# Optimization experiments

Hardware: AMD Instinct MI355X
Metric: run time of the kernel (lower is better)

The kernel has to match this reference:

```python
import jax, jax.numpy as jnp
import numpy as np

B, N, T, F = 8, 2000, 64, 32
H = 128    # lstm_hidden
GH = 128   # gnn_hidden
E = 32000  # edges


def setup_inputs() -> dict:
    key = jax.random.key(0)
    ks = jax.random.split(key, 12)
    s = 0.05
    return {
        "x": jax.random.normal(ks[0], (B, N, T, F), jnp.float32),
        "edge_index": jax.random.randint(ks[1], (2, E), 0, N, dtype=jnp.int32),
        # LSTM params (torch gate order i, f, g, o)
        "Wih": jax.random.normal(ks[2], (4 * H, F), jnp.float32) * s,
        "Whh": jax.random.normal(ks[3], (4 * H, H), jnp.float32) * s,
        "bih": jax.random.normal(ks[4], (4 * H,), jnp.float32) * s,
        "bhh": jax.random.normal(ks[5], (4 * H,), jnp.float32) * s,
        # GCNConv params
        "gcn_W": jax.random.normal(ks[6], (H, GH), jnp.float32) * s,
        "gcn_b": jax.random.normal(ks[7], (GH,), jnp.float32) * s,
        # shared MLP head
        "mlp_W1": jax.random.normal(ks[8], (GH, GH // 2), jnp.float32) * s,
        "mlp_b1": jax.random.normal(ks[9], (GH // 2,), jnp.float32) * s,
        "mlp_W2": jax.random.normal(ks[10], (GH // 2, 1), jnp.float32) * s,
        "mlp_b2": jax.random.normal(ks[11], (1,), jnp.float32) * s,
    }


def _lstm_last_h(x, Wih, Whh, bih, bhh):
    # x: [M, T, F] -> last hidden state [M, H]
    M = x.shape[0]
    xg = jnp.einsum('mtf,gf->mtg', x, Wih) + bih  # precompute input gates [M, T, 4H]

    def step(carry, xg_t):
        h, c = carry
        z = xg_t + h @ Whh.T + bhh
        i, f, g, o = jnp.split(z, 4, axis=-1)
        i = jax.nn.sigmoid(i)
        f = jax.nn.sigmoid(f)
        g = jnp.tanh(g)
        o = jax.nn.sigmoid(o)
        c = f * c + i * g
        h = o * jnp.tanh(c)
        return (h, c), None

    h0 = jnp.zeros((M, H), x.dtype)
    c0 = jnp.zeros((M, H), x.dtype)
    (h, _), _ = jax.lax.scan(step, (h0, c0), jnp.swapaxes(xg, 0, 1))
    return h


def reference(x, edge_index, Wih, Whh, bih, bhh, gcn_W, gcn_b,
              mlp_W1, mlp_b1, mlp_W2, mlp_b2):
    Bx, Nx, Tx, Fx = x.shape
    # LSTM over all B*N node sequences, take last hidden state
    h = _lstm_last_h(x.reshape(Bx * Nx, Tx, Fx), Wih, Whh, bih, bhh)
    node_features = h.reshape(Bx, Nx, H)

    # GCNConv (PyG semantics): add self-loops, symmetric normalization
    loops = jnp.arange(Nx, dtype=edge_index.dtype)
    src = jnp.concatenate([edge_index[0], loops])
    dst = jnp.concatenate([edge_index[1], loops])
    deg = jnp.zeros((Nx,), x.dtype).at[dst].add(1.0)
    dinv = jnp.where(deg > 0, jax.lax.rsqrt(deg), 0.0)
    norm = dinv[src] * dinv[dst]  # [E+N]

    xw = node_features @ gcn_W                     # [B, N, GH]
    msgs = xw[:, src, :] * norm[None, :, None]     # gather + scale [B, E+N, GH]
    agg = jnp.zeros((Bx, Nx, GH), x.dtype).at[:, dst, :].add(msgs) + gcn_b

    # shared MLP head (dropout is identity in eval mode)
    h1 = jax.nn.silu(agg @ mlp_W1 + mlp_b1)
    out = h1 @ mlp_W2 + mlp_b2                     # [B, N, 1]
    return out.squeeze(-1)                         # [B, N]
```

## Files before the change

kernel.cpp:

```cpp
#include <hip/hip_runtime.h>

typedef _Float16 f16x8 __attribute__((ext_vector_type(8)));
typedef _Float16 f16x4 __attribute__((ext_vector_type(4)));
typedef _Float16 f16x2 __attribute__((ext_vector_type(2)));
typedef float f32x4 __attribute__((ext_vector_type(4)));

#define NB_   8
#define NN_   2000
#define TT_   64
#define FF_   32
#define HH_   128
#define EE_   32000
#define KD    160
#define RSTR  192
#define GELEM (32*RSTR)

__device__ __forceinline__ float fexp2(float v) { return __builtin_amdgcn_exp2f(v); }
__device__ __forceinline__ float frcp(float v)  { return __builtin_amdgcn_rcpf(v); }

__global__ void prep_kernel(const float* __restrict__ Wih, const float* __restrict__ Whh,
                            const float* __restrict__ bih, const float* __restrict__ bhh,
                            const float* __restrict__ gcnW,
                            _Float16* __restrict__ W16, _Float16* __restrict__ Wg16,
                            float* __restrict__ bias, float* __restrict__ deg) {
  int idx = blockIdx.x * 256 + threadIdx.x;
  if (idx < 512 * KD) {
    int col = idx / KD, k = idx % KD;
    float v = (k < 32) ? Wih[col * 32 + k] : Whh[col * 128 + (k - 32)];
    float sc = (col >= 256 && col < 384) ? -2.88539008f : -1.44269504f;
    W16[idx] = (_Float16)(v * sc);
  } else if (idx < 512 * KD + 128 * 128) {
    int i2 = idx - 512 * KD;
    int colg = i2 >> 7, k = i2 & 127;
    Wg16[i2] = (_Float16)gcnW[k * 128 + colg];
  } else if (idx < 512 * KD + 128 * 128 + 512) {
    int i3 = idx - (512 * KD + 128 * 128);
    float sc = (i3 >= 256 && i3 < 384) ? -2.88539008f : -1.44269504f;
    bias[i3] = (bih[i3] + bhh[i3]) * sc;
  } else if (idx < 512 * KD + 128 * 128 + 512 + NN_) {
    deg[idx - (512 * KD + 128 * 128 + 512)] = 0.f;
  }
}

__global__ void deg_kernel(const int* __restrict__ ei, float* __restrict__ deg) {
  int e = blockIdx.x * 256 + threadIdx.x;
  if (e < EE_ + NN_) {
    int d = (e < EE_) ? ei[EE_ + e] : (e - EE_);
    atomicAdd(&deg[d], 1.f);
  }
}

__global__ void dinv_kernel(const float* __restrict__ deg, float* __restrict__ dinv) {
  int n = blockIdx.x * 256 + threadIdx.x;
  if (n < NN_) {
    float d = deg[n];
    dinv[n] = (d > 0.f) ? __builtin_amdgcn_rsqf(d) : 0.f;
  }
}

__global__ void scan_kernel(const float* __restrict__ deg, int* __restrict__ offs,
                            int* __restrict__ cursor) {
  __shared__ int s0[2048], s1[2048];
  int t = threadIdx.x;
  for (int i = t; i < 2048; i += 1024) s0[i] = (i < NN_) ? ((int)deg[i] - 1) : 0;
  __syncthreads();
  int* src = s0; int* dst = s1;
  for (int off = 1; off < 2048; off <<= 1) {
    for (int i = t; i < 2048; i += 1024)
      dst[i] = src[i] + ((i >= off) ? src[i - off] : 0);
    __syncthreads();
    int* tmp = src; src = dst; dst = tmp;
  }
  for (int i = t; i < NN_; i += 1024) {
    int exc = src[i] - ((int)deg[i] - 1);
    offs[i] = exc;
    cursor[i] = exc;
  }
}

__global__ void fill_kernel(const int* __restrict__ ei, const float* __restrict__ dinv,
                            int* __restrict__ cursor, int* __restrict__ csr_src,
                            float* __restrict__ csr_w) {
  int e = blockIdx.x * 256 + threadIdx.x;
  if (e >= EE_) return;
  int s = ei[e], d = ei[EE_ + e];
  int pos = atomicAdd(&cursor[d], 1);
  csr_src[pos] = s;
  csr_w[pos] = dinv[s] * dinv[d];
}

__global__ __launch_bounds__(512, 2) void lstm_gcn_kernel(
    const float* __restrict__ x, const _Float16* __restrict__ W16,
    const float* __restrict__ bias, const _Float16* __restrict__ Wg16,
    float* __restrict__ xw) {
  __shared__ _Float16 A[64 * RSTR];
  const int tid  = threadIdx.x;
  const int wave = tid >> 6;
  const int lane = tid & 63;
  const int n15  = lane & 15;
  const int q    = lane >> 4;
  const int m    = n15 & 7;
  const int hm   = m >> 2;
  const int qx   = q ^ (m & 3);
  const int node0 = blockIdx.x * 64;

  f16x8 Af[4][5];
  float4 bgv[4];
#pragma unroll
  for (int g = 0; g < 4; ++g) {
    const int row = g * 128 + wave * 16 + n15;
#pragma unroll
    for (int kc = 0; kc < 5; ++kc)
      Af[g][kc] = *(const f16x8*)(W16 + row * KD + kc * 32 + q * 8);
    bgv[g] = *(const float4*)(bias + g * 128 + wave * 16 + q * 4);
  }

  const int bRow = n15 * RSTR + (qx << 3);
  const int hOff = n15 * RSTR + (((4 + 2 * wave + (q >> 1)) ^ m) << 3) + ((q & 1) << 2);

  const int xrow = tid >> 4;
  const int xf   = (tid & 15) * 2;
  const int xOff = xrow * RSTR + (((xf >> 3) ^ (xrow & 7)) << 3) + (xf & 7);
  const float* xb0 = x + (size_t)(node0 + xrow) * (TT_ * FF_) + xf;
  const float* xb1 = x + (size_t)(node0 + 32 + xrow) * (TT_ * FF_) + xf;

  for (int i = tid; i < 1024; i += 512) {
    int row = i >> 4, ci = i & 15;
    f16x8 z8 = {(_Float16)0, (_Float16)0, (_Float16)0, (_Float16)0,
                (_Float16)0, (_Float16)0, (_Float16)0, (_Float16)0};
    *(f16x8*)(A + row * RSTR + (((4 + ci) ^ (row & 7)) << 3)) = z8;
  }
  {
    float2 v0 = *(const float2*)xb0;
    float2 v1 = *(const float2*)xb1;
    f16x2 p0 = {(_Float16)v0.x, (_Float16)v0.y};
    f16x2 p1 = {(_Float16)v1.x, (_Float16)v1.y};
    *(f16x2*)(A + xOff) = p0;
    *(f16x2*)(A + GELEM + xOff) = p1;
  }
  __syncthreads();

  f32x4 accX[2][4], accY[2][4], cX[2], cY[2];
#pragma unroll
  for (int nt = 0; nt < 2; ++nt) { cX[nt] = (f32x4){0,0,0,0}; cY[nt] = (f32x4){0,0,0,0}; }

  auto mfma_half = [&](int G, int nt, f32x4 (&acc)[4]) {
#pragma unroll
    for (int g = 0; g < 4; ++g)
      acc[g] = (f32x4){bgv[g].x, bgv[g].y, bgv[g].z, bgv[g].w};
#pragma unroll
    for (int kc = 0; kc < 5; ++kc) {
      f16x8 bf = *(const f16x8*)(A + G + nt * (16 * RSTR) + bRow + ((kc ^ hm) << 5));
#pragma unroll
      for (int g = 0; g < 4; ++g)
        acc[g] = __builtin_amdgcn_mfma_f32_16x16x32_f16(Af[g][kc], bf, acc[g], 0, 0, 0);
    }
  };

  auto gates_half = [&](int G, int nt, f32x4 (&acc)[4], f32x4& c) {
    const float EM = 2.68435456e8f;
    float so[4], eC[4], dC[4];
#pragma unroll
    for (int r = 0; r < 4; ++r) {
      float ei = fminf(fexp2(acc[0][r]), EM);
      float ef = fminf(fexp2(acc[1][r]), EM);
      float eg = fminf(fexp2(acc[2][r]), EM);
      float eo = fminf(fexp2(acc[3][r]), EM);
      float di = 1.f + ei, df = 1.f + ef, dg = 1.f + eg, dd = 1.f + eo;
      float p0 = di * df, p1 = dg * dd;
      float rP = frcp(p0 * p1);
      float r0 = rP * p1, r1 = rP * p0;
      float si = r0 * df, sf = r0 * di;
      float tg = 2.f * (r1 * dd) - 1.f;
      so[r] = r1 * dg;
      c[r] = sf * c[r] + si * tg;
    }
#pragma unroll
    for (int r = 0; r < 4; ++r) {
      eC[r] = fminf(fexp2(-2.88539008f * c[r]), EM);
      dC[r] = 1.f + eC[r];
    }
    float q0 = dC[0] * dC[1], q1 = dC[2] * dC[3];
    float rQ = frcp(q0 * q1);
    float s0 = rQ * q1, s1 = rQ * q0;
    f16x4 hp = {(_Float16)(so[0] * (2.f * (s0 * dC[1]) - 1.f)),
                (_Float16)(so[1] * (2.f * (s0 * dC[0]) - 1.f)),
                (_Float16)(so[2] * (2.f * (s1 * dC[3]) - 1.f)),
                (_Float16)(so[3] * (2.f * (s1 * dC[2]) - 1.f))};
    *(f16x4*)(A + G + nt * (16 * RSTR) + hOff) = hp;
  };

  mfma_half(0, 0, accX[0]);
  mfma_half(0, 1, accX[1]);
  __syncthreads();

  for (int t = 0; t < TT_; ++t) {
    const bool more = (t + 1 < TT_);
    {
      float2 xv;
      if (more) xv = *(const float2*)(xb0 + (t + 1) * FF_);
      mfma_half(GELEM, 0, accY[0]);
      gates_half(0, 0, accX[0], cX[0]);
      mfma_half(GELEM, 1, accY[1]);
      gates_half(0, 1, accX[1], cX[1]);
      if (more) { f16x2 p = {(_Float16)xv.x, (_Float16)xv.y}; *(f16x2*)(A + xOff) = p; }
    }
    __syncthreads();
    {
      float2 xv;
      if (more) xv = *(const float2*)(xb1 + (t + 1) * FF_);
      if (more) mfma_half(0, 0, accX[0]);
      gates_half(GELEM, 0, accY[0], cY[0]);
      if (more) mfma_half(0, 1, accX[1]);
      gates_half(GELEM, 1, accY[1], cY[1]);
      if (more) { f16x2 p = {(_Float16)xv.x, (_Float16)xv.y}; *(f16x2*)(A + GELEM + xOff) = p; }
    }
    __syncthreads();
  }

  f16x8 Ag[4];
#pragma unroll
  for (int kc = 0; kc < 4; ++kc)
    Ag[kc] = *(const f16x8*)(Wg16 + (wave * 16 + n15) * HH_ + kc * 32 + q * 8);
  f32x4 acc2[4];
#pragma unroll
  for (int nt = 0; nt < 4; ++nt) acc2[nt] = (f32x4){0, 0, 0, 0};
#pragma unroll
  for (int kc = 0; kc < 4; ++kc)
#pragma unroll
    for (int nt = 0; nt < 4; ++nt) {
      f16x8 bf = *(const f16x8*)(A + (nt * 16 + n15) * RSTR +
                                 (((kc + 1) ^ hm) << 5) + (qx << 3));
      acc2[nt] = __builtin_amdgcn_mfma_f32_16x16x32_f16(Ag[kc], bf, acc2[nt], 0, 0, 0);
    }
#pragma unroll
  for (int nt = 0; nt < 4; ++nt)
    *(float4*)(xw + (size_t)(node0 + nt * 16 + n15) * HH_ + wave * 16 + q * 4) =
        (float4){acc2[nt][0], acc2[nt][1], acc2[nt][2], acc2[nt][3]};
}

__global__ void gathermlp_kernel(const float* __restrict__ xw, const int* __restrict__ offs,
                                 const float* __restrict__ deg, const float* __restrict__ dinv,
                                 const int* __restrict__ csr_src, const float* __restrict__ csr_w,
                                 const float* __restrict__ gcnb,
                                 const float* __restrict__ W1, const float* __restrict__ b1,
                                 const float* __restrict__ W2, const float* __restrict__ b2,
                                 float* __restrict__ out) {
  __shared__ float aggs[8][128];
  const int d = blockIdx.x;
  const int tid = threadIdx.x;
  {
    const int j  = tid & 127;
    const int bh = tid >> 7;
    const int beg = offs[d];
    const int cnt = (int)deg[d] - 1;
    const size_t bbase = (size_t)(bh * 4) * NN_ * 128;
    float a0 = 0.f, a1 = 0.f, a2 = 0.f, a3 = 0.f;
    for (int e = 0; e < cnt; ++e) {
      int s   = csr_src[beg + e];
      float w = csr_w[beg + e];
      const float* p = xw + bbase + (size_t)s * 128 + j;
      a0 += w * p[0];
      a1 += w * p[NN_ * 128];
      a2 += w * p[2 * NN_ * 128];
      a3 += w * p[3 * NN_ * 128];
    }
    {
      float di = dinv[d];
      float w = di * di;
      const float* p = xw + bbase + (size_t)d * 128 + j;
      a0 += w * p[0];
      a1 += w * p[NN_ * 128];
      a2 += w * p[2 * NN_ * 128];
      a3 += w * p[3 * NN_ * 128];
    }
    float bj = gcnb[j];
    aggs[bh * 4 + 0][j] = a0 + bj;
    aggs[bh * 4 + 1][j] = a1 + bj;
    aggs[bh * 4 + 2][j] = a2 + bj;
    aggs[bh * 4 + 3][j] = a3 + bj;
  }
  __syncthreads();
  const int b = tid >> 5;
  const int t = tid & 31;
  float acc1 = b1[t], acc2 = b1[t + 32];
#pragma unroll 4
  for (int k = 0; k < 128; ++k) {
    float a = aggs[b][k];
    acc1 += a * W1[k * 64 + t];
    acc2 += a * W1[k * 64 + t + 32];
  }
  float s1 = acc1 * frcp(1.f + fexp2(-1.44269504f * acc1));
  float s2 = acc2 * frcp(1.f + fexp2(-1.44269504f * acc2));
  float part = s1 * W2[t] + s2 * W2[t + 32];
#pragma unroll
  for (int msk = 16; msk >= 1; msk >>= 1) part += __shfl_xor(part, msk);
  if (t == 0) out[(size_t)b * NN_ + d] = part + b2[0];
}

extern "C" void kernel_launch(void* const* d_in, const int* in_sizes, int n_in,
                              void* d_out, int out_size, void* d_ws, size_t ws_size,
                              hipStream_t stream) {
  const float* x    = (const float*)d_in[0];
  const int*   ei   = (const int*)d_in[1];
  const float* Wih  = (const float*)d_in[2];
  const float* Whh  = (const float*)d_in[3];
  const float* bih  = (const float*)d_in[4];
  const float* bhh  = (const float*)d_in[5];
  const float* gcnW = (const float*)d_in[6];
  const float* gcnb = (const float*)d_in[7];
  const float* W1   = (const float*)d_in[8];
  const float* b1   = (const float*)d_in[9];
  const float* W2   = (const float*)d_in[10];
  const float* b2   = (const float*)d_in[11];
  float* out = (float*)d_out;
  char* ws = (char*)d_ws;

  _Float16* W16    = (_Float16*)(ws);
  _Float16* Wg16   = (_Float16*)(ws + 163840);
  float*    bias   = (float*)(ws + 196608);
  float*    xw     = (float*)(ws + 198656);
  float*    deg    = (float*)(ws + 8390656);
  float*    dinv   = (float*)(ws + 8398848);
  int*      offs   = (int*)(ws + 8407040);
  int*      cursor = (int*)(ws + 8415232);
  int*      csrs   = (int*)(ws + 8423424);
  float*    csrw   = (float*)(ws + 8551424);

  prep_kernel<<<394, 256, 0, stream>>>(Wih, Whh, bih, bhh, gcnW, W16, Wg16, bias, deg);
  deg_kernel<<<133, 256, 0, stream>>>(ei, deg);
  dinv_kernel<<<8, 256, 0, stream>>>(deg, dinv);
  scan_kernel<<<1, 1024, 0, stream>>>(deg, offs, cursor);
  fill_kernel<<<125, 256, 0, stream>>>(ei, dinv, cursor, csrs, csrw);
  lstm_gcn_kernel<<<250, 512, 0, stream>>>(x, W16, bias, Wg16, xw);
  gathermlp_kernel<<<NN_, 256, 0, stream>>>(xw, offs, deg, dinv, csrs, csrw,
                                            gcnb, W1, b1, W2, b2, out);
}
```

Baseline: 423.6 us.

## Halve LSTM nodes per block, move input weights to LDS, transpose xw for gather

The LSTM kernel now handles 32 nodes per block instead of 64 and launches 500 blocks with a higher occupancy target. It drops the two-group ping-pong software pipeline, keeps the input-projection weights and bias in LDS rather than registers, and uses plain per-gate sigmoid/tanh instead of shared-reciprocal tricks. The xw output is stored node-major with batch interleaved so each gather touches one contiguous 4KB row. The MLP gets a transposed W1 in LDS with float4 dot products and an edge loop unrolled by two, and the dinv kernel is folded into the scan kernel. The trade is more waves available to hide latency against losing the explicit MFMA/gate overlap, plus extra per-block LDS traffic for weights and for staging W1.

```diff
diff --git a/kernel.cpp b/kernel.cpp
--- a/kernel.cpp
+++ b/kernel.cpp
@@ -13,7 +13,8 @@
 #define EE_   32000
 #define KD    160
 #define RSTR  192
-#define GELEM (32*RSTR)
+#define NODES 32
+#define WXSTR 40
 
 __device__ __forceinline__ float fexp2(float v) { return __builtin_amdgcn_exp2f(v); }
 __device__ __forceinline__ float frcp(float v)  { return __builtin_amdgcn_rcpf(v); }
@@ -50,16 +51,8 @@
   }
 }
 
-__global__ void dinv_kernel(const float* __restrict__ deg, float* __restrict__ dinv) {
-  int n = blockIdx.x * 256 + threadIdx.x;
-  if (n < NN_) {
-    float d = deg[n];
-    dinv[n] = (d > 0.f) ? __builtin_amdgcn_rsqf(d) : 0.f;
-  }
-}
-
 __global__ void scan_kernel(const float* __restrict__ deg, int* __restrict__ offs,
-                            int* __restrict__ cursor) {
+                            int* __restrict__ cursor, float* __restrict__ dinv) {
   __shared__ int s0[2048], s1[2048];
   int t = threadIdx.x;
   for (int i = t; i < 2048; i += 1024) s0[i] = (i < NN_) ? ((int)deg[i] - 1) : 0;
@@ -75,6 +68,8 @@
     int exc = src[i] - ((int)deg[i] - 1);
     offs[i] = exc;
     cursor[i] = exc;
+    float d = deg[i];
+    dinv[i] = (d > 0.f) ? __builtin_amdgcn_rsqf(d) : 0.f;
   }
 }
 
@@ -89,11 +84,13 @@
   csr_w[pos] = dinv[s] * dinv[d];
 }
 
-__global__ __launch_bounds__(512, 2) void lstm_gcn_kernel(
+__global__ __launch_bounds__(512, 4) void lstm_gcn_kernel(
     const float* __restrict__ x, const _Float16* __restrict__ W16,
     const float* __restrict__ bias, const _Float16* __restrict__ Wg16,
-    float* __restrict__ xw) {
-  __shared__ _Float16 A[64 * RSTR];
+    float* __restrict__ xwT) {
+  __shared__ _Float16 A[NODES * RSTR];
+  __shared__ _Float16 WxL[512 * WXSTR];
+  __shared__ float    BiasL[512];
   const int tid  = threadIdx.x;
   const int wave = tid >> 6;
   const int lane = tid & 63;
@@ -102,119 +99,103 @@
   const int m    = n15 & 7;
   const int hm   = m >> 2;
   const int qx   = q ^ (m & 3);
-  const int node0 = blockIdx.x * 64;
-
-  f16x8 Af[4][5];
-  float4 bgv[4];
+  const int node0 = blockIdx.x * NODES;
+
+  f16x8 Af[4][4];
 #pragma unroll
   for (int g = 0; g < 4; ++g) {
     const int row = g * 128 + wave * 16 + n15;
 #pragma unroll
-    for (int kc = 0; kc < 5; ++kc)
-      Af[g][kc] = *(const f16x8*)(W16 + row * KD + kc * 32 + q * 8);
-    bgv[g] = *(const float4*)(bias + g * 128 + wave * 16 + q * 4);
+    for (int kc = 1; kc < 5; ++kc)
+      Af[g][kc - 1] = *(const f16x8*)(W16 + row * KD + kc * 32 + q * 8);
+  }
+  {
+    const _Float16* wr = W16 + tid * KD;
+#pragma unroll
+    for (int cch = 0; cch < 4; ++cch)
+      *(f16x8*)(WxL + tid * WXSTR + cch * 8) = *(const f16x8*)(wr + cch * 8);
+    if (tid < 128) *(float4*)(BiasL + tid * 4) = *(const float4*)(bias + tid * 4);
   }
 
   const int bRow = n15 * RSTR + (qx << 3);
   const int hOff = n15 * RSTR + (((4 + 2 * wave + (q >> 1)) ^ m) << 3) + ((q & 1) << 2);
+  const int aRow = (wave * 16 + n15) * WXSTR + q * 8;
 
   const int xrow = tid >> 4;
   const int xf   = (tid & 15) * 2;
   const int xOff = xrow * RSTR + (((xf >> 3) ^ (xrow & 7)) << 3) + (xf & 7);
-  const float* xb0 = x + (size_t)(node0 + xrow) * (TT_ * FF_) + xf;
-  const float* xb1 = x + (size_t)(node0 + 32 + xrow) * (TT_ * FF_) + xf;
-
-  for (int i = tid; i < 1024; i += 512) {
-    int row = i >> 4, ci = i & 15;
+  const float* xb = x + (size_t)(node0 + xrow) * (TT_ * FF_) + xf;
+
+  {
+    int row = tid >> 4, ci = tid & 15;
     f16x8 z8 = {(_Float16)0, (_Float16)0, (_Float16)0, (_Float16)0,
                 (_Float16)0, (_Float16)0, (_Float16)0, (_Float16)0};
     *(f16x8*)(A + row * RSTR + (((4 + ci) ^ (row & 7)) << 3)) = z8;
   }
   {
-    float2 v0 = *(const float2*)xb0;
-    float2 v1 = *(const float2*)xb1;
-    f16x2 p0 = {(_Float16)v0.x, (_Float16)v0.y};
-    f16x2 p1 = {(_Float16)v1.x, (_Float16)v1.y};
-    *(f16x2*)(A + xOff) = p0;
-    *(f16x2*)(A + GELEM + xOff) = p1;
+    float2 v = *(const float2*)xb;
+    f16x2 p = {(_Float16)v.x, (_Float16)v.y};
+    *(f16x2*)(A + xOff) = p;
   }
   __syncthreads();
 
-  f32x4 accX[2][4], accY[2][4], cX[2], cY[2];
-#pragma unroll
-  for (int nt = 0; nt < 2; ++nt) { cX[nt] = (f32x4){0,0,0,0}; cY[nt] = (f32x4){0,0,0,0}; }
-
-  auto mfma_half = [&](int G, int nt, f32x4 (&acc)[4]) {
-#pragma unroll
-    for (int g = 0; g < 4; ++g)
-      acc[g] = (f32x4){bgv[g].x, bgv[g].y, bgv[g].z, bgv[g].w};
-#pragma unroll
-    for (int kc = 0; kc < 5; ++kc) {
-      f16x8 bf = *(const f16x8*)(A + G + nt * (16 * RSTR) + bRow + ((kc ^ hm) << 5));
+  f32x4 acc[2][4], c[2];
+  c[0] = (f32x4){0, 0, 0, 0};
+  c[1] = (f32x4){0, 0, 0, 0};
+
+  for (int t = 0; t < TT_; ++t) {
+    {
+      f32x4 bt[4];
 #pragma unroll
       for (int g = 0; g < 4; ++g)
-        acc[g] = __builtin_amdgcn_mfma_f32_16x16x32_f16(Af[g][kc], bf, acc[g], 0, 0, 0);
-    }
-  };
-
-  auto gates_half = [&](int G, int nt, f32x4 (&acc)[4], f32x4& c) {
-    const float EM = 2.68435456e8f;
-    float so[4], eC[4], dC[4];
-#pragma unroll
-    for (int r = 0; r < 4; ++r) {
-      float ei = fminf(fexp2(acc[0][r]), EM);
-      float ef = fminf(fexp2(acc[1][r]), EM);
-      float eg = fminf(fexp2(acc[2][r]), EM);
-      float eo = fminf(fexp2(acc[3][r]), EM);
-      float di = 1.f + ei, df = 1.f + ef, dg = 1.f + eg, dd = 1.f + eo;
-      float p0 = di * df, p1 = dg * dd;
-      float rP = frcp(p0 * p1);
-      float r0 = rP * p1, r1 = rP * p0;
-      float si = r0 * df, sf = r0 * di;
-      float tg = 2.f * (r1 * dd) - 1.f;
-      so[r] = r1 * dg;
-      c[r] = sf * c[r] + si * tg;
-    }
-#pragma unroll
-    for (int r = 0; r < 4; ++r) {
-      eC[r] = fminf(fexp2(-2.88539008f * c[r]), EM);
-      dC[r] = 1.f + eC[r];
-    }
-    float q0 = dC[0] * dC[1], q1 = dC[2] * dC[3];
-    float rQ = frcp(q0 * q1);
-    float s0 = rQ * q1, s1 = rQ * q0;
-    f16x4 hp = {(_Float16)(so[0] * (2.f * (s0 * dC[1]) - 1.f)),
-                (_Float16)(so[1] * (2.f * (s0 * dC[0]) - 1.f)),
-                (_Float16)(so[2] * (2.f * (s1 * dC[3]) - 1.f)),
-                (_Float16)(so[3] * (2.f * (s1 * dC[2]) - 1.f))};
-    *(f16x4*)(A + G + nt * (16 * RSTR) + hOff) = hp;
-  };
-
-  mfma_half(0, 0, accX[0]);
-  mfma_half(0, 1, accX[1]);
-  __syncthreads();
-
-  for (int t = 0; t < TT_; ++t) {
+        bt[g] = *(const f32x4*)(BiasL + g * 128 + wave * 16 + q * 4);
+#pragma unroll
+      for (int nt = 0; nt < 2; ++nt)
+#pragma unroll
+        for (int g = 0; g < 4; ++g) acc[nt][g] = bt[g];
+      f16x8 ax[4];
+#pragma unroll
+      for (int g = 0; g < 4; ++g)
+        ax[g] = *(const f16x8*)(WxL + g * 128 * WXSTR + aRow);
+#pragma unroll
+      for (int nt = 0; nt < 2; ++nt) {
+        f16x8 bf = *(const f16x8*)(A + nt * (16 * RSTR) + bRow + (hm << 5));
+#pragma unroll
+        for (int g = 0; g < 4; ++g)
+          acc[nt][g] = __builtin_amdgcn_mfma_f32_16x16x32_f16(ax[g], bf, acc[nt][g], 0, 0, 0);
+      }
+#pragma unroll
+      for (int kc = 1; kc < 5; ++kc)
+#pragma unroll
+        for (int nt = 0; nt < 2; ++nt) {
+          f16x8 bf = *(const f16x8*)(A + nt * (16 * RSTR) + bRow + ((kc ^ hm) << 5));
+#pragma unroll
+          for (int g = 0; g < 4; ++g)
+            acc[nt][g] = __builtin_amdgcn_mfma_f32_16x16x32_f16(Af[g][kc - 1], bf, acc[nt][g], 0, 0, 0);
+        }
+    }
     const bool more = (t + 1 < TT_);
-    {
-      float2 xv;
-      if (more) xv = *(const float2*)(xb0 + (t + 1) * FF_);
-      mfma_half(GELEM, 0, accY[0]);
-      gates_half(0, 0, accX[0], cX[0]);
-      mfma_half(GELEM, 1, accY[1]);
-      gates_half(0, 1, accX[1], cX[1]);
-      if (more) { f16x2 p = {(_Float16)xv.x, (_Float16)xv.y}; *(f16x2*)(A + xOff) = p; }
-    }
+    float2 xv;
+    if (more) xv = *(const float2*)(xb + (t + 1) * FF_);
     __syncthreads();
-    {
-      float2 xv;
-      if (more) xv = *(const float2*)(xb1 + (t + 1) * FF_);
-      if (more) mfma_half(0, 0, accX[0]);
-      gates_half(GELEM, 0, accY[0], cY[0]);
-      if (more) mfma_half(0, 1, accX[1]);
-      gates_half(GELEM, 1, accY[1], cY[1]);
-      if (more) { f16x2 p = {(_Float16)xv.x, (_Float16)xv.y}; *(f16x2*)(A + GELEM + xOff) = p; }
-    }
+
+#pragma unroll
+    for (int nt = 0; nt < 2; ++nt) {
+      f16x4 hp;
+#pragma unroll
+      for (int r = 0; r < 4; ++r) {
+        float si = frcp(1.f + fexp2(acc[nt][0][r]));
+        float sf = frcp(1.f + fexp2(acc[nt][1][r]));
+        float tg = 2.f * frcp(1.f + fexp2(acc[nt][2][r])) - 1.f;
+        float so = frcp(1.f + fexp2(acc[nt][3][r]));
+        float cn = sf * c[nt][r] + si * tg;
+        c[nt][r] = cn;
+        float tc = 2.f * frcp(1.f + fexp2(-2.88539008f * cn)) - 1.f;
+        hp[r] = (_Float16)(so * tc);
+      }
+      *(f16x4*)(A + nt * (16 * RSTR) + hOff) = hp;
+    }
+    if (more) { f16x2 p = {(_Float16)xv.x, (_Float16)xv.y}; *(f16x2*)(A + xOff) = p; }
     __syncthreads();
   }
 
@@ -222,57 +203,73 @@
 #pragma unroll
   for (int kc = 0; kc < 4; ++kc)
     Ag[kc] = *(const f16x8*)(Wg16 + (wave * 16 + n15) * HH_ + kc * 32 + q * 8);
-  f32x4 acc2[4];
-#pragma unroll
-  for (int nt = 0; nt < 4; ++nt) acc2[nt] = (f32x4){0, 0, 0, 0};
+  f32x4 acc2[2];
+  acc2[0] = (f32x4){0, 0, 0, 0};
+  acc2[1] = (f32x4){0, 0, 0, 0};
 #pragma unroll
   for (int kc = 0; kc < 4; ++kc)
 #pragma unroll
-    for (int nt = 0; nt < 4; ++nt) {
-      f16x8 bf = *(const f16x8*)(A + (nt * 16 + n15) * RSTR +
-                                 (((kc + 1) ^ hm) << 5) + (qx << 3));
+    for (int nt = 0; nt < 2; ++nt) {
+      f16x8 bf = *(const f16x8*)(A + nt * (16 * RSTR) + bRow + (((kc + 1) ^ hm) << 5));
       acc2[nt] = __builtin_amdgcn_mfma_f32_16x16x32_f16(Ag[kc], bf, acc2[nt], 0, 0, 0);
     }
 #pragma unroll
-  for (int nt = 0; nt < 4; ++nt)
-    *(float4*)(xw + (size_t)(node0 + nt * 16 + n15) * HH_ + wave * 16 + q * 4) =
+  for (int nt = 0; nt < 2; ++nt) {
+    int mnode = node0 + nt * 16 + n15;
+    int b = mnode / NN_;
+    int n = mnode - b * NN_;
+    *(float4*)(xwT + ((size_t)n * 8 + b) * HH_ + wave * 16 + q * 4) =
         (float4){acc2[nt][0], acc2[nt][1], acc2[nt][2], acc2[nt][3]};
-}
-
-__global__ void gathermlp_kernel(const float* __restrict__ xw, const int* __restrict__ offs,
-                                 const float* __restrict__ deg, const float* __restrict__ dinv,
-                                 const int* __restrict__ csr_src, const float* __restrict__ csr_w,
-                                 const float* __restrict__ gcnb,
-                                 const float* __restrict__ W1, const float* __restrict__ b1,
-                                 const float* __restrict__ W2, const float* __restrict__ b2,
-                                 float* __restrict__ out) {
+  }
+}
+
+__global__ __launch_bounds__(256) void gathermlp_kernel(
+    const float* __restrict__ xwT, const int* __restrict__ offs,
+    const float* __restrict__ deg, const float* __restrict__ dinv,
+    const int* __restrict__ csr_src, const float* __restrict__ csr_w,
+    const float* __restrict__ gcnb,
+    const float* __restrict__ W1, const float* __restrict__ b1,
+    const float* __restrict__ W2, const float* __restrict__ b2,
+    float* __restrict__ out) {
   __shared__ float aggs[8][128];
+  __shared__ float W1T[64][132];
   const int d = blockIdx.x;
   const int tid = threadIdx.x;
+  for (int i = tid; i < 8192; i += 256) {
+    int k = i >> 6, j = i & 63;
+    W1T[j][k] = W1[i];
+  }
   {
     const int j  = tid & 127;
     const int bh = tid >> 7;
     const int beg = offs[d];
     const int cnt = (int)deg[d] - 1;
-    const size_t bbase = (size_t)(bh * 4) * NN_ * 128;
+    const int boff = bh * 512 + j;
     float a0 = 0.f, a1 = 0.f, a2 = 0.f, a3 = 0.f;
-    for (int e = 0; e < cnt; ++e) {
-      int s   = csr_src[beg + e];
+    int e = 0;
+    for (; e + 1 < cnt; e += 2) {
+      int s0 = csr_src[beg + e],     s1 = csr_src[beg + e + 1];
+      float w0 = csr_w[beg + e],     w1 = csr_w[beg + e + 1];
+      const float* p0 = xwT + (size_t)s0 * 1024 + boff;
+      const float* p1 = xwT + (size_t)s1 * 1024 + boff;
+      float v00 = p0[0], v01 = p0[128], v02 = p0[256], v03 = p0[384];
+      float v10 = p1[0], v11 = p1[128], v12 = p1[256], v13 = p1[384];
+      a0 += w0 * v00 + w1 * v10;
+      a1 += w0 * v01 + w1 * v11;
+      a2 += w0 * v02 + w1 * v12;
+      a3 += w0 * v03 + w1 * v13;
+    }
+    if (e < cnt) {
+      int s = csr_src[beg + e];
       float w = csr_w[beg + e];
-      const float* p = xw + bbase + (size_t)s * 128 + j;
-      a0 += w * p[0];
-      a1 += w * p[NN_ * 128];
-      a2 += w * p[2 * NN_ * 128];
-      a3 += w * p[3 * NN_ * 128];
+      const float* p = xwT + (size_t)s * 1024 + boff;
+      a0 += w * p[0]; a1 += w * p[128]; a2 += w * p[256]; a3 += w * p[384];
     }
     {
       float di = dinv[d];
       float w = di * di;
-      const float* p = xw + bbase + (size_t)d * 128 + j;
-      a0 += w * p[0];
-      a1 += w * p[NN_ * 128];
-      a2 += w * p[2 * NN_ * 128];
-      a3 += w * p[3 * NN_ * 128];
+      const float* p = xwT + (size_t)d * 1024 + boff;
+      a0 += w * p[0]; a1 += w * p[128]; a2 += w * p[256]; a3 += w * p[384];
     }
     float bj = gcnb[j];
     aggs[bh * 4 + 0][j] = a0 + bj;
@@ -284,11 +281,13 @@
   const int b = tid >> 5;
   const int t = tid & 31;
   float acc1 = b1[t], acc2 = b1[t + 32];
-#pragma unroll 4
-  for (int k = 0; k < 128; ++k) {
-    float a = aggs[b][k];
-    acc1 += a * W1[k * 64 + t];
-    acc2 += a * W1[k * 64 + t + 32];
+#pragma unroll 8
+  for (int kc = 0; kc < 32; ++kc) {
+    float4 a  = *(const float4*)&aggs[b][kc * 4];
+    float4 w1 = *(const float4*)&W1T[t][kc * 4];
+    float4 w2 = *(const float4*)&W1T[t + 32][kc * 4];
+    acc1 += a.x * w1.x + a.y * w1.y + a.z * w1.z + a.w * w1.w;
+    acc2 += a.x * w2.x + a.y * w2.y + a.z * w2.z + a.w * w2.w;
   }
   float s1 = acc1 * frcp(1.f + fexp2(-1.44269504f * acc1));
   float s2 = acc2 * frcp(1.f + fexp2(-1.44269504f * acc2));
@@ -319,7 +318,7 @@
   _Float16* W16    = (_Float16*)(ws);
   _Float16* Wg16   = (_Float16*)(ws + 163840);
   float*    bias   = (float*)(ws + 196608);
-  float*    xw     = (float*)(ws + 198656);
+  float*    xwT    = (float*)(ws + 198656);
   float*    deg    = (float*)(ws + 8390656);
   float*    dinv   = (float*)(ws + 8398848);
   int*      offs   = (int*)(ws + 8407040);
@@ -329,10 +328,9 @@
 
   prep_kernel<<<394, 256, 0, stream>>>(Wih, Whh, bih, bhh, gcnW, W16, Wg16, bias, deg);
   deg_kernel<<<133, 256, 0, stream>>>(ei, deg);
-  dinv_kernel<<<8, 256, 0, stream>>>(deg, dinv);
-  scan_kernel<<<1, 1024, 0, stream>>>(deg, offs, cursor);
+  scan_kernel<<<1, 1024, 0, stream>>>(deg, offs, cursor, dinv);
   fill_kernel<<<125, 256, 0, stream>>>(ei, dinv, cursor, csrs, csrw);
-  lstm_gcn_kernel<<<250, 512, 0, stream>>>(x, W16, bias, Wg16, xw);
-  gathermlp_kernel<<<NN_, 256, 0, stream>>>(xw, offs, deg, dinv, csrs, csrw,
+  lstm_gcn_kernel<<<500, 512, 0, stream>>>(x, W16, bias, Wg16, xwT);
+  gathermlp_kernel<<<NN_, 256, 0, stream>>>(xwT, offs, deg, dinv, csrs, csrw,
                                             gcnb, W1, b1, W2, b2, out);
 }
```

Result: faster. 407.9 us (-3.7%).
